# Performance work log

Hardware: AMD Instinct MI355X
Metric: run time of the kernel (lower is better)

Reference implementation:

```python
import jax, jax.numpy as jnp
import numpy as np

N, E = 50000, 800000
F_IN, HID, HEADS, NCLS = 128, 64, 4, 16
NEG_SLOPE = 0.2


def setup_inputs() -> dict:
    key = jax.random.key(0)
    ks = jax.random.split(key, 16)
    def glorot(k, shape):
        fan_in, fan_out = shape[0], shape[-1]
        lim = jnp.sqrt(6.0 / (fan_in + fan_out))
        return jax.random.uniform(k, shape, jnp.float32, -lim, lim)
    x = jax.random.normal(ks[0], (N, F_IN), jnp.float32)
    edge_index = jax.random.randint(ks[1], (2, E), 0, N, dtype=jnp.int64)
    inp = {"x": x, "edge_index": edge_index}
    # layer 1: F_IN -> HID x HEADS (concat)
    inp["W1"] = glorot(ks[2], (F_IN, HEADS * HID))
    inp["a1_src"] = glorot(ks[3], (HEADS, HID))
    inp["a1_dst"] = glorot(ks[4], (HEADS, HID))
    inp["b1"] = jnp.zeros((HEADS * HID,), jnp.float32)
    # layer 2: HEADS*HID -> HID x HEADS (concat)
    inp["W2"] = glorot(ks[5], (HEADS * HID, HEADS * HID))
    inp["a2_src"] = glorot(ks[6], (HEADS, HID))
    inp["a2_dst"] = glorot(ks[7], (HEADS, HID))
    inp["b2"] = jnp.zeros((HEADS * HID,), jnp.float32)
    # layer 3: HEADS*HID -> NCLS, heads=1, concat=False (mean)
    inp["W3"] = glorot(ks[8], (HEADS * HID, NCLS))
    inp["a3_src"] = glorot(ks[9], (1, NCLS))
    inp["a3_dst"] = glorot(ks[10], (1, NCLS))
    inp["b3"] = jnp.zeros((NCLS,), jnp.float32)
    return inp


def gat_conv(x, src, dst, W, a_src, a_dst, b, heads, out_dim, concat):
    n = x.shape[0]
    h = (x @ W).reshape(n, heads, out_dim)           # [N, H, D]
    s_src = jnp.sum(h * a_src, axis=-1)              # [N, H]
    s_dst = jnp.sum(h * a_dst, axis=-1)              # [N, H]
    e = jax.nn.leaky_relu(s_src[src] + s_dst[dst], NEG_SLOPE)  # [E, H]
    # segment softmax over incoming edges of each dst node
    m = jax.ops.segment_max(e, dst, num_segments=n)
    ex = jnp.exp(e - m[dst])
    z = jax.ops.segment_sum(ex, dst, num_segments=n)
    alpha = ex / z[dst]                              # [E, H]
    msg = h[src] * alpha[:, :, None]                 # [E, H, D]
    out = jax.ops.segment_sum(msg, dst, num_segments=n)  # [N, H, D]
    out = out.reshape(n, heads * out_dim) if concat else out.mean(axis=1)
    return out + b


def reference(x, edge_index, W1, a1_src, a1_dst, b1, W2, a2_src, a2_dst, b2,
              W3, a3_src, a3_dst, b3):
    n = x.shape[0]
    loop = jnp.arange(n, dtype=edge_index.dtype)
    src = jnp.concatenate([edge_index[0], loop])     # add self-loops (PyG default)
    dst = jnp.concatenate([edge_index[1], loop])
    h = jax.nn.elu(gat_conv(x, src, dst, W1, a1_src, a1_dst, b1, HEADS, HID, True))
    h = jax.nn.elu(gat_conv(h, src, dst, W2, a2_src, a2_dst, b2, HEADS, HID, True))
    h = gat_conv(h, src, dst, W3, a3_src, a3_dst, b3, 1, NCLS, False)
    return jax.nn.log_softmax(h, axis=1)
```

## Files before the change

### kernel.cpp

```cpp
#include <hip/hip_runtime.h>
#include <hip/hip_bf16.h>
#include <math.h>

#define N_NODES 50000
#define N_EDGES 800000
#define F_IN    128
#define HID     64
#define HEADS   4
#define NCLS    16
#define NEG_SLOPE 0.2f

typedef __attribute__((ext_vector_type(8))) _Float16 half8v;
typedef __attribute__((ext_vector_type(4))) float f32x4;
typedef __attribute__((ext_vector_type(2))) float f32x2;

static __device__ __forceinline__ float lrelu(float x) {
    return x >= 0.f ? x : NEG_SLOPE * x;
}
static __device__ __forceinline__ unsigned short f2h(float f) {
    _Float16 h = (_Float16)f;
    return __builtin_bit_cast(unsigned short, h);
}
static __device__ __forceinline__ float h2f(unsigned short u) {
    return (float)__builtin_bit_cast(_Float16, u);
}

__global__ void k_zero(int4* __restrict__ p, int n4) {
    int i = blockIdx.x * blockDim.x + threadIdx.x;
    if (i < n4) p[i] = int4{0, 0, 0, 0};
}

#define NB_WT1  128
#define NB_WT2  256
#define NB_HIST 3125
__global__ void k_prep(const float* __restrict__ W1, unsigned short* __restrict__ W1t,
                       const float* __restrict__ W2, unsigned short* __restrict__ W2t,
                       const int* __restrict__ dst, int* __restrict__ counts,
                       unsigned short* __restrict__ rank) {
    int bid = blockIdx.x, tid = threadIdx.x;
    if (bid < NB_WT1) {
        int i = bid * 256 + tid;
        int k = i >> 8, c = i & 255;
        W1t[c * F_IN + k] = f2h(W1[i]);
    } else if (bid < NB_WT1 + NB_WT2) {
        int i = (bid - NB_WT1) * 256 + tid;
        int k = i >> 8, c = i & 255;
        W2t[c * 256 + k] = f2h(W2[i]);
    } else {
        int i = (bid - NB_WT1 - NB_WT2) * 256 + tid;
        if (i < N_EDGES) rank[i] = (unsigned short)atomicAdd(&counts[dst[i]], 1);
    }
}

__global__ __launch_bounds__(256) void k_scan1(const int* __restrict__ counts, int* __restrict__ incl,
                                               int* __restrict__ bsums, int n) {
    __shared__ int wsum[4];
    int blk = blockIdx.x, tid = threadIdx.x;
    int lane = tid & 63, w = tid >> 6;
    int i0 = blk * 1024 + tid * 4;
    int v[4];
    #pragma unroll
    for (int j = 0; j < 4; j++) v[j] = (i0 + j < n) ? counts[i0 + j] : 0;
    int t = v[0] + v[1] + v[2] + v[3];
    int x = t;
    #pragma unroll
    for (int d = 1; d < 64; d <<= 1) { int y = __shfl_up(x, d); if (lane >= d) x += y; }
    if (lane == 63) wsum[w] = x;
    __syncthreads();
    int woff = 0;
    #pragma unroll
    for (int ww = 0; ww < 4; ww++) woff += (ww < w) ? wsum[ww] : 0;
    int p = woff + x - t;
    #pragma unroll
    for (int j = 0; j < 4; j++) { p += v[j]; if (i0 + j < n) incl[i0 + j] = p; }
    if (tid == 255) bsums[blk] = woff + x;
}

__global__ void k_scan2(const int* __restrict__ bsums, int* __restrict__ boffs, int nb, int* rowptr_end) {
    int lane = threadIdx.x;
    int v = (lane < nb) ? bsums[lane] : 0;
    int x = v;
    #pragma unroll
    for (int d = 1; d < 64; d <<= 1) { int y = __shfl_up(x, d); if (lane >= d) x += y; }
    if (lane < nb) boffs[lane] = x - v;
    if (lane == 63) *rowptr_end = x;
}

__global__ void k_scan3(const int* __restrict__ incl, const int* __restrict__ counts,
                        const int* __restrict__ boffs, int* __restrict__ rowptr, int n) {
    int i = blockIdx.x * blockDim.x + threadIdx.x;
    if (i < n) rowptr[i] = boffs[i >> 10] + incl[i] - counts[i];
}

static __device__ __forceinline__ int swz(int r, int lc) {
    return r * 4 + (lc ^ (r & 3) ^ ((r >> 2) & 1));
}

template<int CONVA>
static __device__ __forceinline__ void gemm_body(
        int bid, const void* __restrict__ Av, const unsigned short* __restrict__ Bt,
        const float* __restrict__ asrc, const float* __restrict__ adst,
        unsigned char* __restrict__ C8, float* __restrict__ s_src, float* __restrict__ s_dst,
        int M, int K, unsigned short* Asm, unsigned short* Bsm) {
    int tid = threadIdx.x;
    int lane = tid & 63, wid = tid >> 6;
    int bx = bid & 1, by = bid >> 1;
    int row0 = by * 128, col0 = bx * 128;
    int wr = wid >> 1, wc = wid & 1;
    f32x4 acc[4][4] = {};

    for (int k0 = 0; k0 < K; k0 += 32) {
        __syncthreads();
        #pragma unroll
        for (int s = 0; s < 2; s++) {
            int c = tid + s * 256;
            int row = c >> 2, lc = c & 3;
            int gr = row0 + row; if (gr >= M) gr = 0;
            uint4 va;
            if (CONVA) {
                const float* Af = (const float*)Av + (size_t)gr * K + k0 + lc * 8;
                float4 fa = *(const float4*)Af;
                float4 fb = *(const float4*)(Af + 4);
                va.x = (unsigned)f2h(fa.x) | ((unsigned)f2h(fa.y) << 16);
                va.y = (unsigned)f2h(fa.z) | ((unsigned)f2h(fa.w) << 16);
                va.z = (unsigned)f2h(fb.x) | ((unsigned)f2h(fb.y) << 16);
                va.w = (unsigned)f2h(fb.z) | ((unsigned)f2h(fb.w) << 16);
            } else {
                va = *(const uint4*)((const unsigned short*)Av + (size_t)gr * K + k0 + lc * 8);
            }
            *(uint4*)(&Asm[swz(row, lc) * 8]) = va;
            uint4 vb = *(const uint4*)(Bt + (size_t)(col0 + row) * K + k0 + lc * 8);
            *(uint4*)(&Bsm[swz(row, lc) * 8]) = vb;
        }
        __syncthreads();
        half8v af[4], bg[4];
        int lq = lane >> 4;
        #pragma unroll
        for (int m = 0; m < 4; m++) {
            int r = wr * 64 + m * 16 + (lane & 15);
            af[m] = *(const half8v*)(&Asm[swz(r, lq) * 8]);
        }
        #pragma unroll
        for (int n = 0; n < 4; n++) {
            int r = wc * 64 + n * 16 + (lane & 15);
            bg[n] = *(const half8v*)(&Bsm[swz(r, lq) * 8]);
        }
        #pragma unroll
        for (int m = 0; m < 4; m++)
            #pragma unroll
            for (int n = 0; n < 4; n++)
                acc[m][n] = __builtin_amdgcn_mfma_f32_16x16x32_f16(af[m], bg[n], acc[m][n], 0, 0, 0);
    }

    #pragma unroll
    for (int m = 0; m < 4; m++) {
        #pragma unroll
        for (int r = 0; r < 4; r++) {
            int row = row0 + wr * 64 + m * 16 + (lane >> 4) * 4 + r;
            if (row < M) {
                int q01 = __builtin_amdgcn_cvt_pk_fp8_f32(acc[m][0][r], acc[m][1][r], 0, false);
                int q23 = __builtin_amdgcn_cvt_pk_fp8_f32(acc[m][2][r], acc[m][3][r], 0, false);
                size_t base = (size_t)row * 256 + col0 + wc * 64 + (lane & 15);
                C8[base]      = (unsigned char)(q01 & 0xff);
                C8[base + 16] = (unsigned char)((q01 >> 8) & 0xff);
                C8[base + 32] = (unsigned char)(q23 & 0xff);
                C8[base + 48] = (unsigned char)((q23 >> 8) & 0xff);
            }
        }
    }

    int c16 = lane & 15, lq = lane >> 4;
    int head = bx * 2 + wc;
    float avs[4], avd[4];
    #pragma unroll
    for (int nn = 0; nn < 4; nn++) {
        avs[nn] = asrc[head * 64 + nn * 16 + c16];
        avd[nn] = adst[head * 64 + nn * 16 + c16];
    }
    #pragma unroll
    for (int mm = 0; mm < 4; mm++) {
        #pragma unroll
        for (int r = 0; r < 4; r++) {
            float ps = 0.f, pd = 0.f;
            #pragma unroll
            for (int nn = 0; nn < 4; nn++) {
                ps += acc[mm][nn][r] * avs[nn];
                pd += acc[mm][nn][r] * avd[nn];
            }
            #pragma unroll
            for (int off = 1; off < 16; off <<= 1) {
                ps += __shfl_xor(ps, off);
                pd += __shfl_xor(pd, off);
            }
            if (c16 == 0) {
                int grow = row0 + wr * 64 + mm * 16 + lq * 4 + r;
                if (grow < M) {
                    s_src[grow * 4 + head] = ps;
                    s_dst[grow * 4 + head] = pd;
                }
            }
        }
    }
}

__global__ __launch_bounds__(256) void k_gemm_mfma(const unsigned short* __restrict__ A,
                                                   const unsigned short* __restrict__ Bt,
                                                   const float* __restrict__ asrc,
                                                   const float* __restrict__ adst,
                                                   unsigned char* __restrict__ C8,
                                                   float* __restrict__ s_src,
                                                   float* __restrict__ s_dst,
                                                   int M, int K) {
    __shared__ unsigned short Asm[128 * 32];
    __shared__ unsigned short Bsm[128 * 32];
    gemm_body<0>(blockIdx.x, A, Bt, asrc, adst, C8, s_src, s_dst, M, K, Asm, Bsm);
}

__global__ __launch_bounds__(256) void k_b(const float* __restrict__ A,
                                           const unsigned short* __restrict__ Bt,
                                           const float* __restrict__ asrc,
                                           const float* __restrict__ adst,
                                           unsigned char* __restrict__ C8,
                                           float* __restrict__ s_src,
                                           float* __restrict__ s_dst,
                                           int M, int K, int gemmBlocks,
                                           const int* __restrict__ src, const int* __restrict__ dst,
                                           const int* __restrict__ rowptr,
                                           const unsigned short* __restrict__ rank,
                                           unsigned* __restrict__ colp, int e) {
    __shared__ unsigned short Asm[128 * 32];
    __shared__ unsigned short Bsm[128 * 32];
    int bid = blockIdx.x;
    if (bid < gemmBlocks) {
        gemm_body<1>(bid, A, Bt, asrc, adst, C8, s_src, s_dst, M, K, Asm, Bsm);
    } else {
        int half = (e + 1) >> 1;
        int i = (bid - gemmBlocks) * 256 + (int)threadIdx.x;
        if (i < half) {
            int d = dst[i];
            colp[rowptr[d] + rank[i]] = (unsigned)src[i] | ((unsigned)d << 16);
        }
        int j = i + half;
        if (j < e) {
            int d = dst[j];
            colp[rowptr[d] + rank[j]] = (unsigned)src[j] | ((unsigned)d << 16);
        }
    }
}

__global__ void k_aggregate(const unsigned char* __restrict__ h8, const int* __restrict__ rowptr,
                            const unsigned* __restrict__ colp,
                            const float* __restrict__ s_src, const float* __restrict__ s_dst,
                            const float* __restrict__ bias,
                            unsigned short* __restrict__ out, int n, int e) {
    int wave = (blockIdx.x * blockDim.x + threadIdx.x) >> 6;
    int lane = threadIdx.x & 63;
    if (wave >= n) return;
    int half = lane >> 5, l5 = lane & 31;
    int head = l5 >> 3;
    unsigned foff = (unsigned)(l5 * 8);
    int rs = rowptr[wave], re = rowptr[wave + 1];
    float sd = s_dst[wave * 4 + head];

    float z = 0.f;
    f32x2 a01 = {0.f, 0.f}, a23 = {0.f, 0.f}, a45 = {0.f, 0.f}, a67 = {0.f, 0.f};
    #define PEDGE(SV) __expf(fminf(lrelu((SV) + sd), 80.f))
    #define ACC8(P, HV) { \
        f32x2 pbc = {(P), (P)}; \
        f32x2 v0 = __builtin_amdgcn_cvt_pk_f32_fp8((HV).x, false); \
        f32x2 v1 = __builtin_amdgcn_cvt_pk_f32_fp8((HV).x, true);  \
        f32x2 v2 = __builtin_amdgcn_cvt_pk_f32_fp8((HV).y, false); \
        f32x2 v3 = __builtin_amdgcn_cvt_pk_f32_fp8((HV).y, true);  \
        asm("v_pk_fma_f32 %0, %1, %2, %0" : "+v"(a01) : "v"(v0), "v"(pbc)); \
        asm("v_pk_fma_f32 %0, %1, %2, %0" : "+v"(a23) : "v"(v1), "v"(pbc)); \
        asm("v_pk_fma_f32 %0, %1, %2, %0" : "+v"(a45) : "v"(v2), "v"(pbc)); \
        asm("v_pk_fma_f32 %0, %1, %2, %0" : "+v"(a67) : "v"(v3), "v"(pbc)); \
        z += (P); }

    if (half == 0) {
        float pself = PEDGE(s_src[wave * 4 + head]);
        uint2 own = *(const uint2*)(h8 + (((unsigned)wave << 8) + foff));
        ACC8(pself, own);
    }
    int i = rs + half;
    for (; i + 14 < re; i += 16) {
        unsigned cc[8]; float sv[8]; uint2 hv[8];
        #pragma unroll
        for (int j = 0; j < 8; j++) cc[j] = colp[i + 2 * j];
        #pragma unroll
        for (int j = 0; j < 8; j++) sv[j] = s_src[(cc[j] & 0xffffu) * 4 + head];
        #pragma unroll
        for (int j = 0; j < 8; j++)
            hv[j] = *(const uint2*)(h8 + (((cc[j] & 0xffffu) << 8) + foff));
        #pragma unroll
        for (int j = 0; j < 8; j++) {
            float p = PEDGE(sv[j]);
            ACC8(p, hv[j]);
        }
    }
    for (; i + 6 < re; i += 8) {
        unsigned cc[4]; float sv[4]; uint2 hv[4];
        #pragma unroll
        for (int j = 0; j < 4; j++) cc[j] = colp[i + 2 * j];
        #pragma unroll
        for (int j = 0; j < 4; j++) sv[j] = s_src[(cc[j] & 0xffffu) * 4 + head];
        #pragma unroll
        for (int j = 0; j < 4; j++)
            hv[j] = *(const uint2*)(h8 + (((cc[j] & 0xffffu) << 8) + foff));
        #pragma unroll
        for (int j = 0; j < 4; j++) {
            float p = PEDGE(sv[j]);
            ACC8(p, hv[j]);
        }
    }
    for (; i < re; i += 2) {
        unsigned c0 = colp[i];
        float s0 = s_src[(c0 & 0xffffu) * 4 + head];
        uint2 h0 = *(const uint2*)(h8 + (((c0 & 0xffffu) << 8) + foff));
        float p0 = PEDGE(s0);
        ACC8(p0, h0);
    }
    #undef ACC8
    #undef PEDGE
    z += __shfl_xor(z, 32);
    float a[8] = {a01.x, a01.y, a23.x, a23.y, a45.x, a45.y, a67.x, a67.y};
    #pragma unroll
    for (int j = 0; j < 8; j++) a[j] += __shfl_xor(a[j], 32);

    if (half == 0) {
        float inv = 1.f / z;
        int f0 = l5 * 8;
        float4 bv0 = *(const float4*)(bias + f0);
        float4 bv1 = *(const float4*)(bias + f0 + 4);
        float o[8];
        o[0] = a[0] * inv + bv0.x; o[1] = a[1] * inv + bv0.y;
        o[2] = a[2] * inv + bv0.z; o[3] = a[3] * inv + bv0.w;
        o[4] = a[4] * inv + bv1.x; o[5] = a[5] * inv + bv1.y;
        o[6] = a[6] * inv + bv1.z; o[7] = a[7] * inv + bv1.w;
        #pragma unroll
        for (int j = 0; j < 8; j++) o[j] = o[j] > 0.f ? o[j] : __expf(o[j]) - 1.f;
        uint4 ov;
        unsigned* w = (unsigned*)&ov;
        #pragma unroll
        for (int j = 0; j < 4; j++)
            w[j] = (unsigned)f2h(o[2 * j]) | ((unsigned)f2h(o[2 * j + 1]) << 16);
        *(uint4*)(out + (size_t)wave * 256 + f0) = ov;
    }
}

__global__ __launch_bounds__(256) void k_gemm3(const unsigned short* __restrict__ A,
                                               const float* __restrict__ B,
                                               const float* __restrict__ a3s,
                                               const float* __restrict__ a3d,
                                               float* __restrict__ C,
                                               float* __restrict__ s_src,
                                               float* __restrict__ s_dst,
                                               int M, int K) {
    __shared__ float Bs[256 * 16];
    for (int i = threadIdx.x; i < K * 16; i += 256) Bs[i] = B[i];
    __syncthreads();
    int tx = threadIdx.x & 15;
    int ty = threadIdx.x >> 4;
    int row = blockIdx.x * 16 + ty;
    if (row >= M) return;
    const unsigned short* Ar = A + (size_t)row * K;
    float acc = 0.f;
    for (int kk = 0; kk < K; kk += 8) {
        uint4 va = *(const uint4*)(Ar + kk);
        const unsigned* u = (const unsigned*)&va;
        #pragma unroll
        for (int j = 0; j < 4; j++) {
            float lo = h2f((unsigned short)(u[j] & 0xffff));
            float hi = h2f((unsigned short)(u[j] >> 16));
            acc += lo * Bs[(kk + 2 * j) * 16 + tx] + hi * Bs[(kk + 2 * j + 1) * 16 + tx];
        }
    }
    C[(size_t)row * 16 + tx] = acc;
    float ps = acc * a3s[tx], pd = acc * a3d[tx];
    #pragma unroll
    for (int off = 1; off < 16; off <<= 1) {
        ps += __shfl_xor(ps, off);
        pd += __shfl_xor(pd, off);
    }
    if (tx == 0) { s_src[row] = ps; s_dst[row] = pd; }
}

__global__ void k_agg3(const float* __restrict__ h3, const int* __restrict__ rowptr,
                       const unsigned* __restrict__ colp,
                       const float* __restrict__ s_src, const float* __restrict__ s_dst,
                       const float* __restrict__ b3,
                       float* __restrict__ outp, int n) {
    int wave = (blockIdx.x * blockDim.x + threadIdx.x) >> 6;
    int lane = threadIdx.x & 63;
    if (wave >= n) return;
    int g = lane >> 4, c = lane & 15;
    int rs = rowptr[wave], re = rowptr[wave + 1];
    float sdn = s_dst[wave];

    float z = 0.f, acc = 0.f;
    if (g == 0) {
        float p = __expf(fminf(lrelu(s_src[wave] + sdn), 80.f));
        z += p;
        acc += p * h3[(size_t)wave * 16 + c];
    }
    int i = rs + g;
    for (; i + 12 < re; i += 16) {
        int s0 = colp[i] & 0xffff,     s1 = colp[i + 4] & 0xffff;
        int s2 = colp[i + 8] & 0xffff, s3 = colp[i + 12] & 0xffff;
        float q0 = s_src[s0], q1 = s_src[s1], q2 = s_src[s2], q3 = s_src[s3];
        float v0 = h3[(size_t)s0 * 16 + c], v1 = h3[(size_t)s1 * 16 + c];
        float v2 = h3[(size_t)s2 * 16 + c], v3 = h3[(size_t)s3 * 16 + c];
        float p0 = __expf(fminf(lrelu(q0 + sdn), 80.f));
        float p1 = __expf(fminf(lrelu(q1 + sdn), 80.f));
        float p2 = __expf(fminf(lrelu(q2 + sdn), 80.f));
        float p3 = __expf(fminf(lrelu(q3 + sdn), 80.f));
        z += (p0 + p1) + (p2 + p3);
        acc += p0 * v0 + p1 * v1 + p2 * v2 + p3 * v3;
    }
    for (; i + 4 < re; i += 8) {
        int s0 = colp[i] & 0xffff, s1 = colp[i + 4] & 0xffff;
        float q0 = s_src[s0], q1 = s_src[s1];
        float v0 = h3[(size_t)s0 * 16 + c], v1 = h3[(size_t)s1 * 16 + c];
        float p0 = __expf(fminf(lrelu(q0 + sdn), 80.f));
        float p1 = __expf(fminf(lrelu(q1 + sdn), 80.f));
        z += p0 + p1;
        acc += p0 * v0 + p1 * v1;
    }
    for (; i < re; i += 4) {
        int s = colp[i] & 0xffff;
        float p = __expf(fminf(lrelu(s_src[s] + sdn), 80.f));
        z += p;
        acc += p * h3[(size_t)s * 16 + c];
    }
    z += __shfl_xor(z, 16);  z += __shfl_xor(z, 32);
    acc += __shfl_xor(acc, 16); acc += __shfl_xor(acc, 32);
    if (lane < 16) {
        float v = acc / z + b3[c];
        float mm = v;
        #pragma unroll
        for (int off = 1; off < 16; off <<= 1) mm = fmaxf(mm, __shfl_xor(mm, off));
        float se = __expf(v - mm);
        #pragma unroll
        for (int off = 1; off < 16; off <<= 1) se += __shfl_xor(se, off);
        outp[(size_t)wave * 16 + c] = v - mm - logf(se);
    }
}

extern "C" void kernel_launch(void* const* d_in, const int* in_sizes, int n_in,
                              void* d_out, int out_size, void* d_ws, size_t ws_size,
                              hipStream_t stream) {
    const float* x      = (const float*)d_in[0];
    const int*   ei     = (const int*)d_in[1];
    const float* W1     = (const float*)d_in[2];
    const float* a1_src = (const float*)d_in[3];
    const float* a1_dst = (const float*)d_in[4];
    const float* b1     = (const float*)d_in[5];
    const float* W2     = (const float*)d_in[6];
    const float* a2_src = (const float*)d_in[7];
    const float* a2_dst = (const float*)d_in[8];
    const float* b2     = (const float*)d_in[9];
    const float* W3     = (const float*)d_in[10];
    const float* a3_src = (const float*)d_in[11];
    const float* a3_dst = (const float*)d_in[12];
    const float* b3     = (const float*)d_in[13];
    float* outp = (float*)d_out;

    const int N = N_NODES, E = N_EDGES;
    const int* src = ei;
    const int* dst = ei + E;

    char* ws = (char*)d_ws;
    size_t off = 0;
    auto alloc = [&](size_t bytes) {
        void* p = ws + off;
        off = (off + bytes + 255) & ~(size_t)255;
        return p;
    };
    int*   rowptr = (int*)alloc((N + 1) * sizeof(int));
    int*   counts = (int*)alloc(N * sizeof(int));
    unsigned* colp = (unsigned*)alloc(E * sizeof(unsigned));
    unsigned short* rank = (unsigned short*)alloc(E * sizeof(short));
    int*   incl   = (int*)alloc(N * sizeof(int));
    int*   bsums  = (int*)alloc(64 * sizeof(int));
    int*   boffs  = (int*)alloc(64 * sizeof(int));
    float* s_src  = (float*)alloc((size_t)N * HEADS * sizeof(float));
    float* s_dst  = (float*)alloc((size_t)N * HEADS * sizeof(float));
    unsigned short* W1t = (unsigned short*)alloc((size_t)256 * F_IN * sizeof(short));
    unsigned short* W2t = (unsigned short*)alloc((size_t)256 * 256 * sizeof(short));
    unsigned char* hA8  = (unsigned char*)alloc((size_t)N * 256);
    unsigned short* hB  = (unsigned short*)alloc((size_t)N * 256 * sizeof(short));
    float* h3     = (float*)alloc((size_t)N * 16 * sizeof(float));
    (void)ws_size;

    const int aggBlocks = (N + 3) / 4;
    const int gemmBlocks = ((N + 127) / 128) * 2;
    const int scatBlocks = ((E + 1) / 2 + 255) / 256;

    k_zero<<<(N / 4 + 255) / 256, 256, 0, stream>>>((int4*)counts, N / 4);
    k_prep<<<NB_WT1 + NB_WT2 + NB_HIST, 256, 0, stream>>>(W1, W1t, W2, W2t, dst, counts, rank);

    const int nb = (N + 1023) / 1024;
    k_scan1<<<nb, 256, 0, stream>>>(counts, incl, bsums, N);
    k_scan2<<<1, 64, 0, stream>>>(bsums, boffs, nb, rowptr + N);
    k_scan3<<<(N + 255) / 256, 256, 0, stream>>>(incl, counts, boffs, rowptr, N);

    k_b<<<gemmBlocks + scatBlocks, 256, 0, stream>>>(x, W1t, a1_src, a1_dst, hA8, s_src, s_dst,
                                                     N, F_IN, gemmBlocks,
                                                     src, dst, rowptr, rank, colp, E);
    k_aggregate<<<aggBlocks, 256, 0, stream>>>(hA8, rowptr, colp, s_src, s_dst, b1, hB, N, E);
    k_gemm_mfma<<<gemmBlocks, 256, 0, stream>>>(hB, W2t, a2_src, a2_dst, hA8, s_src, s_dst, N, 256);
    k_aggregate<<<aggBlocks, 256, 0, stream>>>(hA8, rowptr, colp, s_src, s_dst, b2, hB, N, E);
    k_gemm3<<<(N + 15) / 16, 256, 0, stream>>>(hB, W3, a3_src, a3_dst, h3, s_src, s_dst, N, 256);
    k_agg3<<<aggBlocks, 256, 0, stream>>>(h3, rowptr, colp, s_src, s_dst, b3, outp, N);
}
```

Measured before the change: 231.0 us.

## Share edge attention weights via shuffles and store layer-3 features as fp16

In the layer-1/2 aggregation, each lane now loads and exponentiates the score of only one edge in its 8-lane head group, and the other lanes get that weight through cross-lane shuffles. This replaces eight gathers of s_src and eight exps per lane. The intent is fewer scattered loads and less transcendental work, paid for with extra shuffle instructions. Separately, the layer-3 GEMM output is stored as fp16 instead of fp32, which halves the gather traffic in k_agg3 at the cost of some precision.

New measurement: 229.8 us. About the same (-0.5%).

```diff
diff --git a/kernel.cpp b/kernel.cpp
--- a/kernel.cpp
+++ b/kernel.cpp
@@ -258,6 +258,8 @@
     if (wave >= n) return;
     int half = lane >> 5, l5 = lane & 31;
     int head = l5 >> 3;
+    int j8 = l5 & 7;
+    int base8 = lane & ~7;
     unsigned foff = (unsigned)(l5 * 8);
     int rs = rowptr[wave], re = rowptr[wave + 1];
     float sd = s_dst[wave * 4 + head];
@@ -284,34 +286,36 @@
     }
     int i = rs + half;
     for (; i + 14 < re; i += 16) {
-        unsigned cc[8]; float sv[8]; uint2 hv[8];
+        unsigned cc[8];
         #pragma unroll
         for (int j = 0; j < 8; j++) cc[j] = colp[i + 2 * j];
-        #pragma unroll
-        for (int j = 0; j < 8; j++) sv[j] = s_src[(cc[j] & 0xffffu) * 4 + head];
+        float s_own = s_src[(cc[j8] & 0xffffu) * 4 + head];
+        uint2 hv[8];
         #pragma unroll
         for (int j = 0; j < 8; j++)
             hv[j] = *(const uint2*)(h8 + (((cc[j] & 0xffffu) << 8) + foff));
-        #pragma unroll
-        for (int j = 0; j < 8; j++) {
-            float p = PEDGE(sv[j]);
-            ACC8(p, hv[j]);
-        }
+        float p_own = PEDGE(s_own);
+        float pv[8];
+        #pragma unroll
+        for (int j = 0; j < 8; j++) pv[j] = __shfl(p_own, base8 + j);
+        #pragma unroll
+        for (int j = 0; j < 8; j++) { ACC8(pv[j], hv[j]); }
     }
     for (; i + 6 < re; i += 8) {
-        unsigned cc[4]; float sv[4]; uint2 hv[4];
+        unsigned cc[4];
         #pragma unroll
         for (int j = 0; j < 4; j++) cc[j] = colp[i + 2 * j];
-        #pragma unroll
-        for (int j = 0; j < 4; j++) sv[j] = s_src[(cc[j] & 0xffffu) * 4 + head];
+        float s_own = s_src[(cc[j8 & 3] & 0xffffu) * 4 + head];
+        uint2 hv[4];
         #pragma unroll
         for (int j = 0; j < 4; j++)
             hv[j] = *(const uint2*)(h8 + (((cc[j] & 0xffffu) << 8) + foff));
-        #pragma unroll
-        for (int j = 0; j < 4; j++) {
-            float p = PEDGE(sv[j]);
-            ACC8(p, hv[j]);
-        }
+        float p_own = PEDGE(s_own);
+        float pv[4];
+        #pragma unroll
+        for (int j = 0; j < 4; j++) pv[j] = __shfl(p_own, base8 + j);
+        #pragma unroll
+        for (int j = 0; j < 4; j++) { ACC8(pv[j], hv[j]); }
     }
     for (; i < re; i += 2) {
         unsigned c0 = colp[i];
@@ -352,7 +356,7 @@
                                                const float* __restrict__ B,
                                                const float* __restrict__ a3s,
                                                const float* __restrict__ a3d,
-                                               float* __restrict__ C,
+                                               unsigned short* __restrict__ C,
                                                float* __restrict__ s_src,
                                                float* __restrict__ s_dst,
                                                int M, int K) {
@@ -375,7 +379,7 @@
             acc += lo * Bs[(kk + 2 * j) * 16 + tx] + hi * Bs[(kk + 2 * j + 1) * 16 + tx];
         }
     }
-    C[(size_t)row * 16 + tx] = acc;
+    C[(size_t)row * 16 + tx] = f2h(acc);
     float ps = acc * a3s[tx], pd = acc * a3d[tx];
     #pragma unroll
     for (int off = 1; off < 16; off <<= 1) {
@@ -385,7 +389,7 @@
     if (tx == 0) { s_src[row] = ps; s_dst[row] = pd; }
 }
 
-__global__ void k_agg3(const float* __restrict__ h3, const int* __restrict__ rowptr,
+__global__ void k_agg3(const unsigned short* __restrict__ h3, const int* __restrict__ rowptr,
                        const unsigned* __restrict__ colp,
                        const float* __restrict__ s_src, const float* __restrict__ s_dst,
                        const float* __restrict__ b3,
@@ -401,15 +405,15 @@
     if (g == 0) {
         float p = __expf(fminf(lrelu(s_src[wave] + sdn), 80.f));
         z += p;
-        acc += p * h3[(size_t)wave * 16 + c];
+        acc += p * h2f(h3[(size_t)wave * 16 + c]);
     }
     int i = rs + g;
     for (; i + 12 < re; i += 16) {
         int s0 = colp[i] & 0xffff,     s1 = colp[i + 4] & 0xffff;
         int s2 = colp[i + 8] & 0xffff, s3 = colp[i + 12] & 0xffff;
         float q0 = s_src[s0], q1 = s_src[s1], q2 = s_src[s2], q3 = s_src[s3];
-        float v0 = h3[(size_t)s0 * 16 + c], v1 = h3[(size_t)s1 * 16 + c];
-        float v2 = h3[(size_t)s2 * 16 + c], v3 = h3[(size_t)s3 * 16 + c];
+        float v0 = h2f(h3[(size_t)s0 * 16 + c]), v1 = h2f(h3[(size_t)s1 * 16 + c]);
+        float v2 = h2f(h3[(size_t)s2 * 16 + c]), v3 = h2f(h3[(size_t)s3 * 16 + c]);
         float p0 = __expf(fminf(lrelu(q0 + sdn), 80.f));
         float p1 = __expf(fminf(lrelu(q1 + sdn), 80.f));
         float p2 = __expf(fminf(lrelu(q2 + sdn), 80.f));
@@ -420,7 +424,7 @@
     for (; i + 4 < re; i += 8) {
         int s0 = colp[i] & 0xffff, s1 = colp[i + 4] & 0xffff;
         float q0 = s_src[s0], q1 = s_src[s1];
-        float v0 = h3[(size_t)s0 * 16 + c], v1 = h3[(size_t)s1 * 16 + c];
+        float v0 = h2f(h3[(size_t)s0 * 16 + c]), v1 = h2f(h3[(size_t)s1 * 16 + c]);
         float p0 = __expf(fminf(lrelu(q0 + sdn), 80.f));
         float p1 = __expf(fminf(lrelu(q1 + sdn), 80.f));
         z += p0 + p1;
@@ -430,7 +434,7 @@
         int s = colp[i] & 0xffff;
         float p = __expf(fminf(lrelu(s_src[s] + sdn), 80.f));
         z += p;
-        acc += p * h3[(size_t)s * 16 + c];
+        acc += p * h2f(h3[(size_t)s * 16 + c]);
     }
     z += __shfl_xor(z, 16);  z += __shfl_xor(z, 32);
     acc += __shfl_xor(acc, 16); acc += __shfl_xor(acc, 32);
@@ -489,7 +493,7 @@
     unsigned short* W2t = (unsigned short*)alloc((size_t)256 * 256 * sizeof(short));
     unsigned char* hA8  = (unsigned char*)alloc((size_t)N * 256);
     unsigned short* hB  = (unsigned short*)alloc((size_t)N * 256 * sizeof(short));
-    float* h3     = (float*)alloc((size_t)N * 16 * sizeof(float));
+    unsigned short* h3  = (unsigned short*)alloc((size_t)N * 16 * sizeof(short));
     (void)ws_size;
 
     const int aggBlocks = (N + 3) / 4;
```
